# Performance work log

Hardware: AMD Instinct MI355X
Metric: run time of the kernel (lower is better)

The kernel has to match this reference:

```python
import jax, jax.numpy as jnp
from jax import lax
import numpy as np

# dims
B, S, IN, E = 2, 2048, 512, 1024
INNER = 2 * E              # mLSTM up-projection, proj_factor = 2.0
NH = 4                     # mLSTM cell heads
DH = INNER // NH           # 512
QKV_BLK = 4                # qkv_proj_blocksize
NHW = INNER // QKV_BLK     # heads of block-diagonal (headwise) q/k/v projections
K = 4                      # causal conv1d kernel size
EPS = 1e-6                 # mLSTM cell eps
LN_EPS = 1e-5


def setup_inputs() -> dict:
    key = jax.random.key(0)
    ks = jax.random.split(key, 16)
    n = lambda k, shp, s=0.02: jax.random.normal(k, shp, jnp.float32) * s
    z = lambda shp: jnp.zeros(shp, jnp.float32)
    return dict(
        x=jax.random.normal(ks[0], (B, S, IN), jnp.float32),
        w_in=n(ks[1], (IN, E)), b_in=z((E,)),
        ln1_w=jnp.ones((E,), jnp.float32),
        w_up=n(ks[2], (E, 2 * INNER)), b_up=z((2 * INNER,)),
        conv_w=n(ks[3], (INNER, K), 0.1), conv_b=z((INNER,)),
        q_w=n(ks[4], (NHW, QKV_BLK, QKV_BLK), 0.3), q_b=z((INNER,)),
        k_w=n(ks[5], (NHW, QKV_BLK, QKV_BLK), 0.3), k_b=z((INNER,)),
        v_w=n(ks[6], (NHW, QKV_BLK, QKV_BLK), 0.3), v_b=z((INNER,)),
        ig_w=n(ks[7], (3 * INNER, NH)), ig_b=z((NH,)),
        fg_w=n(ks[8], (3 * INNER, NH)), fg_b=jnp.ones((NH,), jnp.float32),
        onorm_w=jnp.ones((INNER,), jnp.float32),
        skip=n(ks[9], (INNER,), 1.0),
        w_down=n(ks[10], (INNER, E)), b_down=z((E,)),
        post_w=jnp.ones((E,), jnp.float32),
    )


def _layernorm(x, w, eps=LN_EPS):
    m = x.mean(-1, keepdims=True)
    v = x.var(-1, keepdims=True)
    return (x - m) / jnp.sqrt(v + eps) * w


def _headwise(x, w, b):
    # block-diagonal linear: x (B,S,INNER) split into NHW blocks of QKV_BLK
    Bx, Sx, _ = x.shape
    y = jnp.einsum('bshd,hod->bsho', x.reshape(Bx, Sx, NHW, QKV_BLK), w)
    return y.reshape(Bx, Sx, INNER) + b


def _mlstm_parallel(q, k, v, ig, fg):
    # q,k,v: (B,NH,S,DH); ig,fg: (B,NH,S). Parallel (stabilized) mLSTM.
    log_f = jax.nn.log_sigmoid(fg)                       # (B,NH,S)
    cum = jnp.cumsum(log_f, axis=-1)                     # inclusive cumsum
    dmat = cum[..., :, None] - cum[..., None, :]         # F_i - F_j  (B,NH,S,S)
    mask = jnp.tril(jnp.ones((S, S), bool))
    logD = jnp.where(mask, dmat + ig[..., None, :], -jnp.inf)
    m = logD.max(-1, keepdims=True)                      # (B,NH,S,1)
    Dm = jnp.exp(logD - m)
    qk = jnp.einsum('bnid,bnjd->bnij', q, k) / jnp.sqrt(jnp.float32(DH))
    C = qk * Dm
    norm = jnp.maximum(jnp.abs(C.sum(-1, keepdims=True)), jnp.exp(-m))
    return jnp.einsum('bnij,bnjd->bnid', C / (norm + EPS), v)


def _forward(x, w_in, b_in, ln1_w, w_up, b_up, conv_w, conv_b,
             q_w, q_b, k_w, k_b, v_w, v_b, ig_w, ig_b, fg_w, fg_b,
             onorm_w, skip, w_down, b_down, post_w):
    h_in = x @ w_in + b_in                               # (B,S,E); dropout = identity (eval)

    # --- mLSTM block: residual + pre-LN ---
    xn = _layernorm(h_in, ln1_w)
    up = xn @ w_up + b_up                                # (B,S,2*INNER)
    x_m, z = jnp.split(up, 2, axis=-1)

    # causal depthwise conv1d + SiLU
    rhs = conv_w.T[:, None, :]                           # (K,1,INNER)
    xc = lax.conv_general_dilated(x_m, rhs, window_strides=(1,),
                                  padding=[(K - 1, 0)],
                                  dimension_numbers=('NHC', 'HIO', 'NHC'),
                                  feature_group_count=INNER) + conv_b
    x_conv_act = jax.nn.silu(xc)

    q = _headwise(x_conv_act, q_w, q_b)                  # (B,S,INNER)
    k = _headwise(x_conv_act, k_w, k_b)
    v = _headwise(x_m, v_w, v_b)

    if_in = jnp.concatenate([q, k, v], axis=-1)          # (B,S,3*INNER)
    ig = (if_in @ ig_w + ig_b).transpose(0, 2, 1)        # (B,NH,S)
    fg = (if_in @ fg_w + fg_b).transpose(0, 2, 1)

    to_heads = lambda t: t.reshape(B, S, NH, DH).transpose(0, 2, 1, 3)
    h = _mlstm_parallel(to_heads(q), to_heads(k), to_heads(v), ig, fg)  # (B,NH,S,DH)

    # multi-head (group) norm over DH, then learned scale over flat features
    hn = (h - h.mean(-1, keepdims=True)) / jnp.sqrt(h.var(-1, keepdims=True) + LN_EPS)
    hn = hn.transpose(0, 2, 1, 3).reshape(B, S, INNER) * onorm_w

    h_skip = hn + skip * x_conv_act                      # learnable skip
    h_gated = h_skip * jax.nn.silu(z)                    # output gate
    y = h_gated @ w_down + b_down                        # (B,S,E)

    out = h_in + y                                       # residual
    return _layernorm(out, post_w)                       # post_blocks_norm


def reference(x, w_in, b_in, ln1_w, w_up, b_up, conv_w, conv_b,
              q_w, q_b, k_w, k_b, v_w, v_b, ig_w, ig_b, fg_w, fg_b,
              onorm_w, skip, w_down, b_down, post_w):
    return _forward(x, w_in, b_in, ln1_w, w_up, b_up, conv_w, conv_b,
                    q_w, q_b, k_w, k_b, v_w, v_b, ig_w, ig_b, fg_w, fg_b,
                    onorm_w, skip, w_down, b_down, post_w)
```

## Files before the change

### kernel.cpp

```cpp
#include <hip/hip_runtime.h>
#include <hip/hip_bf16.h>

typedef __hip_bfloat16 bf16;
typedef float floatx4 __attribute__((ext_vector_type(4)));
typedef short bf16x8 __attribute__((ext_vector_type(8)));

#define B_      2
#define S_      2048
#define IN_     512
#define E_      1024
#define INNER_  2048
#define NH_     4
#define DH_     512
#define T_      (B_*S_)
#define EPS_CELL 1e-6f
#define LN_EPS_  1e-5f
#define LS      72
#define CTB_    4

__device__ inline float b2f(bf16 x){ return __bfloat162float(x); }
__device__ inline bf16  f2b(float x){ return __float2bfloat16(x); }
__device__ inline float u2f(unsigned int u){ union{unsigned int i; float f;} v; v.i = u; return v.f; }
__device__ inline unsigned short f2bu(float x){ bf16 t = __float2bfloat16(x); unsigned short r; __builtin_memcpy(&r,&t,2); return r; }
__device__ inline void unpack8(uint4 u, float* f){
  f[0]=u2f(u.x<<16); f[1]=u2f(u.x&0xffff0000u);
  f[2]=u2f(u.y<<16); f[3]=u2f(u.y&0xffff0000u);
  f[4]=u2f(u.z<<16); f[5]=u2f(u.z&0xffff0000u);
  f[6]=u2f(u.w<<16); f[7]=u2f(u.w&0xffff0000u);
}
__device__ inline uint4 pack8(const float* f){
  uint4 u;
  u.x = (unsigned)f2bu(f[0]) | ((unsigned)f2bu(f[1])<<16);
  u.y = (unsigned)f2bu(f[2]) | ((unsigned)f2bu(f[3])<<16);
  u.z = (unsigned)f2bu(f[4]) | ((unsigned)f2bu(f[5])<<16);
  u.w = (unsigned)f2bu(f[6]) | ((unsigned)f2bu(f[7])<<16);
  return u;
}
__device__ inline void stv(bf16* p, float v){ *p = f2b(v); }
__device__ inline void stv(float* p, float v){ *p = v; }

typedef __attribute__((address_space(3))) unsigned int lds_u32_t;
typedef __attribute__((address_space(1))) const unsigned int glb_u32_t;
__device__ __forceinline__ void cp_async16(const bf16* g, short* l){
  __builtin_amdgcn_global_load_lds((glb_u32_t*)(const void*)g,
                                   (lds_u32_t*)(void*)l, 16, 0, 0);
}
__device__ __forceinline__ int so_(int row, int c8){ return row*64 + (((c8) ^ (row&7))<<3); }
__device__ __forceinline__ int eo_(int row, int ch){ return row*128 + (((ch) ^ (row&15))<<3); }

#define STAGE_ASYNC(dst, srcbase, stride, kk) \
  { int slot_ = (kk)*256 + tid; int r_ = slot_>>3; int c8_ = (slot_&7) ^ (r_&7); \
    cp_async16((srcbase) + (size_t)r_*(stride) + c8_*8, &dst[slot_*8]); }

#define STAGE_ASYNC5(dst, srcbase, stride, kk) \
  { int slot_ = (kk)*512 + tid; int r_ = slot_>>3; int c8_ = (slot_&7) ^ (r_&7); \
    cp_async16((srcbase) + (size_t)r_*(stride) + c8_*8, &dst[slot_*8]); }

#define VMWAIT8() asm volatile("s_waitcnt vmcnt(8)" ::: "memory")
#define VMWAIT6() asm volatile("s_waitcnt vmcnt(6)" ::: "memory")
#define VMWAIT0() asm volatile("s_waitcnt vmcnt(0)" ::: "memory")
#define RAWBAR()  do { asm volatile("" ::: "memory"); __builtin_amdgcn_s_barrier(); asm volatile("" ::: "memory"); } while(0)

__device__ inline void transpose_tile(const float* W, bf16* Wt, int K, int N,
    int n0, int k0, int tid, float (*tl)[65]){
  #pragma unroll
  for (int i=0;i<4;i++){
    int idx = tid + i*256; int r = idx>>4, c4 = idx&15;
    float4 v = *(const float4*)(W + (size_t)(k0+r)*N + n0 + c4*4);
    tl[r][c4*4+0]=v.x; tl[r][c4*4+1]=v.y; tl[r][c4*4+2]=v.z; tl[r][c4*4+3]=v.w;
  }
  __syncthreads();
  #pragma unroll
  for (int i=0;i<4;i++){
    int idx = tid + i*256; int rn = idx>>4, c4 = idx&15;
    ushort4 o;
    o.x=f2bu(tl[c4*4+0][rn]); o.y=f2bu(tl[c4*4+1][rn]);
    o.z=f2bu(tl[c4*4+2][rn]); o.w=f2bu(tl[c4*4+3][rn]);
    *(ushort4*)(Wt + (size_t)(n0+rn)*K + k0 + c4*4) = o;
  }
}

__global__ __launch_bounds__(256) void prep_fused(const float* __restrict__ x,
    const float* __restrict__ w_in, const float* __restrict__ w_up,
    const float* __restrict__ igw, const float* __restrict__ fgw,
    bf16* __restrict__ xbf, bf16* __restrict__ w_in_t, bf16* __restrict__ w_up_t,
    bf16* __restrict__ gwb){
  __shared__ float tl[64][65];
  int bid = blockIdx.x, tid = threadIdx.x;
  if (bid < 1024){
    int i = bid*256 + tid;
    const float4* p = (const float4*)(x) + i*2;
    float4 a = p[0], b = p[1];
    ushort4 o0, o1;
    o0.x=f2bu(a.x); o0.y=f2bu(a.y); o0.z=f2bu(a.z); o0.w=f2bu(a.w);
    o1.x=f2bu(b.x); o1.y=f2bu(b.y); o1.z=f2bu(b.z); o1.w=f2bu(b.w);
    ushort4* q = (ushort4*)(xbf) + i*2;
    q[0]=o0; q[1]=o1;
  } else if (bid < 1152){
    int id = bid - 1024;
    int n0 = (id & 15)*64, k0 = (id >> 4)*64;
    transpose_tile(w_in, w_in_t, IN_, E_, n0, k0, tid, tl);
  } else if (bid < 2176){
    int id = bid - 1152;
    int n0 = (id & 63)*64, k0 = (id >> 6)*64;
    transpose_tile(w_up, w_up_t, E_, 2*INNER_, n0, k0, tid, tl);
  } else {
    int idx = (bid - 2176)*256 + tid;
    if (idx < 3*INNER_){
      int g = idx >> 9;
      int e = (idx >> 6) & 7;
      int l = idx & 63;
      int r = g*512 + l*8 + e;
      float4 a = *(const float4*)(igw + (size_t)r*4);
      float4 b = *(const float4*)(fgw + (size_t)r*4);
      ushort4 o0, o1;
      o0.x=f2bu(a.x); o0.y=f2bu(a.y); o0.z=f2bu(a.z); o0.w=f2bu(a.w);
      o1.x=f2bu(b.x); o1.y=f2bu(b.y); o1.z=f2bu(b.z); o1.w=f2bu(b.w);
      *(ushort4*)(gwb + (size_t)idx*8)     = o0;
      *(ushort4*)(gwb + (size_t)idx*8 + 4) = o1;
    }
  }
}

__global__ __launch_bounds__(256) void mfma_gemm(const bf16* __restrict__ A,
    const bf16* __restrict__ Bt, const float* __restrict__ bias, bf16* __restrict__ C,
    int Kd, int lda, int ldc, int NN){
  int bid = blockIdx.x;
  int MM = gridDim.x / NN;
  int mPerX = MM >> 3;
  int xcd = bid & 7, seq = bid >> 3;
  int nb = seq % NN, mb = xcd*mPerX + seq / NN;
  int n0 = nb*128, m0 = mb*128;
  __shared__ __align__(16) short smem[32768];
  int tid = threadIdx.x;
  int w = tid>>6, l = tid&63, lq = l>>4, lr = l&15;
  int wm = (w>>1)*64, wn = (w&1)*64;
  const bf16* Abase = A + (size_t)m0*lda;
  const bf16* Bbase = Bt + (size_t)n0*Kd;
  floatx4 acc[4][4];
  #pragma unroll
  for (int mi=0;mi<4;mi++){
    #pragma unroll
    for (int ni=0;ni<4;ni++) acc[mi][ni] = (floatx4){0.f,0.f,0.f,0.f};
  }
  short* As0 = smem;          short* Bs0 = smem + 8192;
  short* As1 = smem + 16384;  short* Bs1 = smem + 24576;
  int NT = Kd >> 6;
  #pragma unroll
  for (int kk=0;kk<4;kk++){
    STAGE_ASYNC(As0, Abase, lda, kk);
    STAGE_ASYNC(Bs0, Bbase, Kd, kk);
  }
  #pragma unroll
  for (int kk=0;kk<4;kk++){
    STAGE_ASYNC(As1, Abase + 64, lda, kk);
    STAGE_ASYNC(Bs1, Bbase + 64, Kd, kk);
  }
  for (int t=0; t<NT; ++t){
    if (t < NT-1) { VMWAIT8(); } else { VMWAIT0(); }
    RAWBAR();
    short* As = (t&1) ? As1 : As0;
    short* Bs = (t&1) ? Bs1 : Bs0;
    #pragma unroll
    for (int ks=0; ks<2; ks++){
      bf16x8 af[4], bfr[4];
      #pragma unroll
      for (int mi=0;mi<4;mi++) af[mi] = *(const bf16x8*)&As[so_(wm+mi*16+lr, ks*4+lq)];
      #pragma unroll
      for (int ni=0;ni<4;ni++) bfr[ni] = *(const bf16x8*)&Bs[so_(wn+ni*16+lr, ks*4+lq)];
      #pragma unroll
      for (int mi=0;mi<4;mi++){
        #pragma unroll
        for (int ni=0;ni<4;ni++)
          acc[mi][ni] = __builtin_amdgcn_mfma_f32_16x16x32_bf16(af[mi], bfr[ni], acc[mi][ni], 0,0,0);
      }
    }
    RAWBAR();
    if (t+2 < NT){
      int k0 = (t+2)*64;
      #pragma unroll
      for (int kk=0;kk<4;kk++){
        STAGE_ASYNC(As, Abase + k0, lda, kk);
        STAGE_ASYNC(Bs, Bbase + k0, Kd, kk);
      }
    }
  }
  float bb[4];
  #pragma unroll
  for (int ni=0;ni<4;ni++) bb[ni] = bias[n0 + wn + ni*16 + lr];
  __syncthreads();
  #pragma unroll
  for (int mi=0;mi<4;mi++){
    #pragma unroll
    for (int ni=0;ni<4;ni++){
      int coll = wn + ni*16 + lr;
      int ch = coll>>3, off = coll&7;
      #pragma unroll
      for (int r=0;r<4;r++){
        int rowl = wm + mi*16 + lq*4 + r;
        smem[rowl*128 + (((ch) ^ (rowl&15))<<3) + off] = (short)f2bu(acc[mi][ni][r] + bb[ni]);
      }
    }
  }
  __syncthreads();
  #pragma unroll
  for (int i=0;i<8;i++){
    int slot = i*256 + tid;
    int r = slot >> 4, c8 = slot & 15;
    uint4 val = *(const uint4*)&smem[eo_(r, c8)];
    *(uint4*)(C + (size_t)(m0+r)*ldc + n0 + c8*8) = val;
  }
}

__global__ __launch_bounds__(256) void mfma_gemm64(const bf16* __restrict__ A,
    const bf16* __restrict__ Bt, const float* __restrict__ bias, bf16* __restrict__ C,
    int Kd, int lda, int ldc, int NN){
  int bid = blockIdx.x;
  int MM = gridDim.x / NN;
  int mPerX = MM >> 3;
  int xcd = bid & 7, seq = bid >> 3;
  int nb = seq % NN, mb = xcd*mPerX + seq / NN;
  int n0 = nb*128, m0 = mb*64;
  __shared__ __align__(16) short smem[24576];
  int tid = threadIdx.x;
  int w = tid>>6, l = tid&63, lq = l>>4, lr = l&15;
  int wm = (w>>1)*32, wn = (w&1)*64;
  const bf16* Abase = A + (size_t)m0*lda;
  const bf16* Bbase = Bt + (size_t)n0*Kd;
  floatx4 acc[2][4];
  #pragma unroll
  for (int mi=0;mi<2;mi++){
    #pragma unroll
    for (int ni=0;ni<4;ni++) acc[mi][ni] = (floatx4){0.f,0.f,0.f,0.f};
  }
  short* As0 = smem;          short* Bs0 = smem + 4096;
  short* As1 = smem + 12288;  short* Bs1 = smem + 16384;
  int NT = Kd >> 6;
  STAGE_ASYNC(As0, Abase, lda, 0);
  STAGE_ASYNC(As0, Abase, lda, 1);
  #pragma unroll
  for (int kk=0;kk<4;kk++){ STAGE_ASYNC(Bs0, Bbase, Kd, kk); }
  STAGE_ASYNC(As1, Abase + 64, lda, 0);
  STAGE_ASYNC(As1, Abase + 64, lda, 1);
  #pragma unroll
  for (int kk=0;kk<4;kk++){ STAGE_ASYNC(Bs1, Bbase + 64, Kd, kk); }
  for (int t=0; t<NT; ++t){
    if (t < NT-1) { VMWAIT6(); } else { VMWAIT0(); }
    RAWBAR();
    short* As = (t&1) ? As1 : As0;
    short* Bs = (t&1) ? Bs1 : Bs0;
    #pragma unroll
    for (int ks=0; ks<2; ks++){
      bf16x8 af[2], bfr[4];
      #pragma unroll
      for (int mi=0;mi<2;mi++) af[mi] = *(const bf16x8*)&As[so_(wm+mi*16+lr, ks*4+lq)];
      #pragma unroll
      for (int ni=0;ni<4;ni++) bfr[ni] = *(const bf16x8*)&Bs[so_(wn+ni*16+lr, ks*4+lq)];
      #pragma unroll
      for (int mi=0;mi<2;mi++){
        #pragma unroll
        for (int ni=0;ni<4;ni++)
          acc[mi][ni] = __builtin_amdgcn_mfma_f32_16x16x32_bf16(af[mi], bfr[ni], acc[mi][ni], 0,0,0);
      }
    }
    RAWBAR();
    if (t+2 < NT){
      int k0 = (t+2)*64;
      STAGE_ASYNC(As, Abase + k0, lda, 0);
      STAGE_ASYNC(As, Abase + k0, lda, 1);
      #pragma unroll
      for (int kk=0;kk<4;kk++){ STAGE_ASYNC(Bs, Bbase + k0, Kd, kk); }
    }
  }
  float bb[4];
  #pragma unroll
  for (int ni=0;ni<4;ni++) bb[ni] = bias[n0 + wn + ni*16 + lr];
  __syncthreads();
  #pragma unroll
  for (int mi=0;mi<2;mi++){
    #pragma unroll
    for (int ni=0;ni<4;ni++){
      int coll = wn + ni*16 + lr;
      int ch = coll>>3, off = coll&7;
      #pragma unroll
      for (int r=0;r<4;r++){
        int rowl = wm + mi*16 + lq*4 + r;
        smem[rowl*128 + (((ch) ^ (rowl&15))<<3) + off] = (short)f2bu(acc[mi][ni][r] + bb[ni]);
      }
    }
  }
  __syncthreads();
  #pragma unroll
  for (int i=0;i<4;i++){
    int slot = i*256 + tid;
    int r = slot >> 4, c8 = slot & 15;
    uint4 val = *(const uint4*)&smem[eo_(r, c8)];
    *(uint4*)(C + (size_t)(m0+r)*ldc + n0 + c8*8) = val;
  }
}

template<typename OutT>
__global__ __launch_bounds__(256) void ln_rows(const bf16* __restrict__ X,
    const bf16* __restrict__ Xadd, const float* __restrict__ w, OutT* __restrict__ Y){
  int row = blockIdx.x, tid = threadIdx.x;
  size_t base = (size_t)row*E_;
  float vals[4], s=0.f, s2=0.f;
  #pragma unroll
  for (int e=0;e<4;e++){
    int c = e*256+tid;
    float v = b2f(X[base+c]);
    if (Xadd) v += b2f(Xadd[base+c]);
    vals[e]=v; s+=v; s2+=v*v;
  }
  __shared__ float sa[256], sb[256];
  sa[tid]=s; sb[tid]=s2; __syncthreads();
  for (int off=128; off>0; off>>=1){
    if (tid<off){ sa[tid]+=sa[tid+off]; sb[tid]+=sb[tid+off]; }
    __syncthreads();
  }
  float mean = sa[0]*(1.f/E_);
  float var  = sb[0]*(1.f/E_) - mean*mean;
  float rstd = rsqrtf(var + LN_EPS_);
  #pragma unroll
  for (int e=0;e<4;e++){
    int c = e*256+tid;
    stv(&Y[base+c], (vals[e]-mean)*rstd*w[c]);
  }
}

__global__ __launch_bounds__(256) void conv_headwise(const bf16* __restrict__ up,
    const float* __restrict__ cw, const float* __restrict__ cb,
    const float* __restrict__ qw, const float* __restrict__ qb,
    const float* __restrict__ kw, const float* __restrict__ kb,
    const float* __restrict__ vw, const float* __restrict__ vb,
    bf16* __restrict__ xca, bf16* __restrict__ q, bf16* __restrict__ k,
    bf16* __restrict__ v){
  int t0 = blockIdx.x*CTB_;
  int s0 = t0 & (S_-1);
  int c0 = threadIdx.x*8;
  int hw0 = c0 >> 2;

  float row[7][8];
  #pragma unroll
  for (int j=0;j<7;j++){
    if (s0-3+j >= 0){
      uint4 rv = *(const uint4*)(up + (size_t)(t0-3+j)*(2*INNER_) + c0);
      unpack8(rv, row[j]);
    } else {
      #pragma unroll
      for (int e=0;e<8;e++) row[j][e]=0.f;
    }
  }

  float xc[CTB_][8];
  {
    float cwv[8][4], cbv[8];
    #pragma unroll
    for (int e=0;e<8;e++){
      float4 w4 = *(const float4*)(cw + (size_t)(c0+e)*4);
      cwv[e][0]=w4.x; cwv[e][1]=w4.y; cwv[e][2]=w4.z; cwv[e][3]=w4.w;
    }
    float4 b0 = *(const float4*)(cb+c0), b1 = *(const float4*)(cb+c0+4);
    cbv[0]=b0.x; cbv[1]=b0.y; cbv[2]=b0.z; cbv[3]=b0.w;
    cbv[4]=b1.x; cbv[5]=b1.y; cbv[6]=b1.z; cbv[7]=b1.w;
    #pragma unroll
    for (int i=0;i<CTB_;i++){
      #pragma unroll
      for (int e=0;e<8;e++){
        float a = cbv[e];
        #pragma unroll
        for (int t=0;t<4;t++) a += row[i+t][e]*cwv[e][t];
        xc[i][e] = a/(1.f+expf(-a));
      }
      *(uint4*)(xca + (size_t)(t0+i)*INNER_ + c0) = pack8(xc[i]);
    }
  }

  {
    float wv_[32], bv[8];
    #pragma unroll
    for (int g=0;g<2;g++){
      #pragma unroll
      for (int r4=0;r4<4;r4++){
        float4 w4 = *(const float4*)(vw + (size_t)(hw0+g)*16 + r4*4);
        wv_[g*16+r4*4+0]=w4.x; wv_[g*16+r4*4+1]=w4.y;
        wv_[g*16+r4*4+2]=w4.z; wv_[g*16+r4*4+3]=w4.w;
      }
    }
    float4 b0 = *(const float4*)(vb+c0), b1 = *(const float4*)(vb+c0+4);
    bv[0]=b0.x; bv[1]=b0.y; bv[2]=b0.z; bv[3]=b0.w;
    bv[4]=b1.x; bv[5]=b1.y; bv[6]=b1.z; bv[7]=b1.w;
    #pragma unroll
    for (int i=0;i<CTB_;i++){
      float ov[8];
      #pragma unroll
      for (int g=0;g<2;g++){
        #pragma unroll
        for (int o=0;o<4;o++){
          float a = bv[g*4+o];
          #pragma unroll
          for (int d=0;d<4;d++) a += row[i+3][g*4+d]*wv_[g*16+o*4+d];
          ov[g*4+o]=a;
        }
      }
      *(uint4*)(v + (size_t)(t0+i)*INNER_ + c0) = pack8(ov);
    }
  }

  {
    float wv_[32], bv[8];
    #pragma unroll
    for (int g=0;g<2;g++){
      #pragma unroll
      for (int r4=0;r4<4;r4++){
        float4 w4 = *(const float4*)(qw + (size_t)(hw0+g)*16 + r4*4);
        wv_[g*16+r4*4+0]=w4.x; wv_[g*16+r4*4+1]=w4.y;
        wv_[g*16+r4*4+2]=w4.z; wv_[g*16+r4*4+3]=w4.w;
      }
    }
    float4 b0 = *(const float4*)(qb+c0), b1 = *(const float4*)(qb+c0+4);
    bv[0]=b0.x; bv[1]=b0.y; bv[2]=b0.z; bv[3]=b0.w;
    bv[4]=b1.x; bv[5]=b1.y; bv[6]=b1.z; bv[7]=b1.w;
    #pragma unroll
    for (int i=0;i<CTB_;i++){
      float ov[8];
      #pragma unroll
      for (int g=0;g<2;g++){
        #pragma unroll
        for (int o=0;o<4;o++){
          float a = bv[g*4+o];
          #pragma unroll
          for (int d=0;d<4;d++) a += xc[i][g*4+d]*wv_[g*16+o*4+d];
          ov[g*4+o]=a;
        }
      }
      *(uint4*)(q + (size_t)(t0+i)*INNER_ + c0) = pack8(ov);
    }
  }

  {
    float wv_[32], bv[8];
    #pragma unroll
    for (int g=0;g<2;g++){
      #pragma unroll
      for (int r4=0;r4<4;r4++){
        float4 w4 = *(const float4*)(kw + (size_t)(hw0+g)*16 + r4*4);
        wv_[g*16+r4*4+0]=w4.x; wv_[g*16+r4*4+1]=w4.y;
        wv_[g*16+r4*4+2]=w4.z; wv_[g*16+r4*4+3]=w4.w;
      }
    }
    float4 b0 = *(const float4*)(kb+c0), b1 = *(const float4*)(kb+c0+4);
    bv[0]=b0.x; bv[1]=b0.y; bv[2]=b0.z; bv[3]=b0.w;
    bv[4]=b1.x; bv[5]=b1.y; bv[6]=b1.z; bv[7]=b1.w;
    #pragma unroll
    for (int i=0;i<CTB_;i++){
      float ov[8];
      #pragma unroll
      for (int g=0;g<2;g++){
        #pragma unroll
        for (int o=0;o<4;o++){
          float a = bv[g*4+o];
          #pragma unroll
          for (int d=0;d<4;d++) a += xc[i][g*4+d]*wv_[g*16+o*4+d];
          ov[g*4+o]=a;
        }
      }
      *(uint4*)(k + (size_t)(t0+i)*INNER_ + c0) = pack8(ov);
    }
  }
}

__global__ __launch_bounds__(256) void gates_transv(const bf16* __restrict__ q,
    const bf16* __restrict__ k, const bf16* __restrict__ v,
    const bf16* __restrict__ gwb, const float* __restrict__ igb,
    const float* __restrict__ fgb, float* __restrict__ igo, float* __restrict__ fgo,
    bf16* __restrict__ vT){
  __shared__ float red[4*32];
  __shared__ short tl[64*LS];
  int bid = blockIdx.x, tid = threadIdx.x;
  if (bid < 512){
    int w = tid >> 6, l = tid & 63;
    int quad = w >> 1, kh = w & 1;
    int tok0 = bid*8 + quad*4;
    float acc[4][8];
    #pragma unroll
    for (int t=0;t<4;t++){
      #pragma unroll
      for (int n=0;n<8;n++) acc[t][n]=0.f;
    }
    #pragma unroll 2
    for (int it=0; it<6; ++it){
      int src = it >> 1, j = it & 1;
      const bf16* sp = (src==0) ? q : ((src==1) ? k : v);
      int pos = kh*1024 + j*512 + l*8;
      int g = src*4 + kh*2 + j;
      uint4 dv[4];
      #pragma unroll
      for (int t=0;t<4;t++)
        dv[t] = *(const uint4*)(sp + (size_t)(tok0+t)*INNER_ + pos);
      float d[4][8];
      #pragma unroll
      for (int t=0;t<4;t++) unpack8(dv[t], d[t]);
      const bf16* wb = gwb + (size_t)g*512*8;
      #pragma unroll
      for (int e=0;e<8;e++){
        uint4 wv = *(const uint4*)(wb + (size_t)(e*64 + l)*8);
        float w8[8]; unpack8(wv, w8);
        #pragma unroll
        for (int t=0;t<4;t++){
          #pragma unroll
          for (int n=0;n<8;n++) acc[t][n] += d[t][e]*w8[n];
        }
      }
    }
    #pragma unroll
    for (int off=1; off<64; off<<=1){
      #pragma unroll
      for (int t=0;t<4;t++){
        #pragma unroll
        for (int n=0;n<8;n++) acc[t][n] += __shfl_xor(acc[t][n], off);
      }
    }
    if (l == 0){
      #pragma unroll
      for (int t=0;t<4;t++){
        #pragma unroll
        for (int n=0;n<8;n++) red[w*32 + t*8 + n] = acc[t][n];
      }
    }
    __syncthreads();
    if (tid < 64){
      int qd = tid >> 5, tn = tid & 31;
      int t = tn >> 3, n = tn & 7;
      float val = red[(qd*2)*32 + tn] + red[(qd*2+1)*32 + tn];
      int tok = bid*8 + qd*4 + t;
      int b = tok >> 11, s = tok & (S_-1);
      if (n < 4) igo[((size_t)(b*NH_+n))*S_ + s] = val + igb[n];
      else       fgo[((size_t)(b*NH_+(n-4)))*S_ + s] = val + fgb[n-4];
    }
  } else {
    int id = bid - 512;
    int sb = id & 31, db = (id >> 5) & 7, h = id >> 8;
    int b = h >> 2, n = h & 3;
    int s0 = sb*64, d0 = db*64;
    #pragma unroll
    for (int i=0;i<2;i++){
      int vv = tid + i*256; int r = vv>>3, c8 = vv&7;
      uint4 x = *(const uint4*)(v + (size_t)(b*S_+s0+r)*INNER_ + n*DH_ + d0 + c8*8);
      *(uint4*)&tl[r*LS + c8*8] = x;
    }
    __syncthreads();
    #pragma unroll
    for (int i=0;i<2;i++){
      int vv = tid + i*256; int r = vv>>3, c8 = vv&7;
      unsigned short tmp[8];
      #pragma unroll
      for (int e=0;e<8;e++) tmp[e] = (unsigned short)tl[(c8*8+e)*LS + r];
      uint4 o; __builtin_memcpy(&o, tmp, 16);
      *(uint4*)(vT + ((size_t)h*DH_ + d0 + r)*S_ + s0 + c8*8) = o;
    }
  }
}

__global__ __launch_bounds__(256) void scan8(const float* __restrict__ igp,
    const float* __restrict__ fgp, float* __restrict__ ap,
    float* __restrict__ Mp, float* __restrict__ flp, float* __restrict__ rowsum){
  int h = blockIdx.x, tid = threadIdx.x;
  const float* fg = fgp + (size_t)h*S_;
  const float* ig = igp + (size_t)h*S_;
  int base = tid*8;
  float loc[8], run = 0.f;
  #pragma unroll
  for (int e=0;e<8;e++){
    float x = fg[base+e];
    float ls = fminf(x,0.f) - log1pf(expf(-fabsf(x)));
    run += ls; loc[e] = run;
  }
  __shared__ float sd[256];
  sd[tid]=run; __syncthreads();
  if (tid==0){ float r=0.f; for(int t=0;t<256;t++){ float t0=sd[t]; sd[t]=r; r+=t0; } }
  __syncthreads();
  float off = sd[tid];
  float lm[8], rm = -3e38f;
  #pragma unroll
  for (int e=0;e<8;e++){
    float F = loc[e]+off; loc[e]=F;
    float aj = ig[base+e]-F;
    ap[(size_t)h*S_+base+e]=aj;
    rm = fmaxf(rm, aj); lm[e]=rm;
  }
  __syncthreads();
  sd[tid]=rm; __syncthreads();
  if (tid==0){ float r=-3e38f; for(int t=0;t<256;t++){ float t0=sd[t]; sd[t]=r; r=fmaxf(r,t0); } }
  __syncthreads();
  float offm = sd[tid];
  #pragma unroll
  for (int e=0;e<8;e++){
    float M = fmaxf(lm[e], offm);
    Mp[(size_t)h*S_+base+e]=M;
    flp[(size_t)h*S_+base+e]=expf(-loc[e]-M);
    rowsum[(size_t)h*S_+base+e]=0.f;
  }
}

__global__ __launch_bounds__(512) void qk_decay_kernel(const bf16* __restrict__ qg,
    const bf16* __restrict__ kg, const float* __restrict__ ap,
    const float* __restrict__ Mp, float* __restrict__ rowsum, bf16* __restrict__ W){
  int h = blockIdx.x & 7;
  int t = 271 - (blockIdx.x >> 3);
  int p = (int)((sqrtf(4.f*t+1.f)-1.f)*0.5f);
  while ((p+1)*(p+2) <= t) p++;
  while (p*(p+1) > t) p--;
  int r0 = t - p*(p+1);
  int nj = p + 1;
  int it = 2*p + (r0 >= nj ? 1 : 0);
  int tj = r0 >= nj ? r0 - nj : r0;
  int b = h >> 2, n = h & 3;
  int i0 = it*64, j0 = tj*128;
  __shared__ __align__(16) short smem[2*12288];
  __shared__ float a_s[128], m_s[64];
  int tid = threadIdx.x;
  if (tid < 128) a_s[tid] = ap[(size_t)h*S_ + j0 + tid];
  if (tid < 64)  m_s[tid] = Mp[(size_t)h*S_ + i0 + tid];
  int w = tid>>6, l = tid&63, lq = l>>4, lr = l&15;
  int wm = (w>>1)*16, wn = (w&1)*64;
  const bf16* Qbase = qg + (size_t)(b*S_+i0)*INNER_ + n*DH_;
  const bf16* Kbase = kg + (size_t)(b*S_+j0)*INNER_ + n*DH_;
  floatx4 acc[4];
  #pragma unroll
  for (int ni=0;ni<4;ni++) acc[ni] = (floatx4){0.f,0.f,0.f,0.f};
  short* Qs0 = smem;          short* Ks0 = smem + 4096;
  short* Qs1 = smem + 12288;  short* Ks1 = smem + 16384;
  STAGE_ASYNC5(Qs0, Qbase, INNER_, 0);
  STAGE_ASYNC5(Ks0, Kbase, INNER_, 0);
  STAGE_ASYNC5(Ks0, Kbase, INNER_, 1);
  __syncthreads();
  const int NT = DH_/64;
  for (int tt=0; tt<NT; ++tt){
    short* Qs  = (tt&1) ? Qs1 : Qs0;
    short* Ks  = (tt&1) ? Ks1 : Ks0;
    short* Qsn = (tt&1) ? Qs0 : Qs1;
    short* Ksn = (tt&1) ? Ks0 : Ks1;
    if (tt+1 < NT){
      int d0 = (tt+1)*64;
      STAGE_ASYNC5(Qsn, Qbase + d0, INNER_, 0);
      STAGE_ASYNC5(Ksn, Kbase + d0, INNER_, 0);
      STAGE_ASYNC5(Ksn, Kbase + d0, INNER_, 1);
    }
    #pragma unroll
    for (int ks=0; ks<2; ks++){
      bf16x8 af, bfr[4];
      af = *(const bf16x8*)&Qs[so_(wm+lr, ks*4+lq)];
      #pragma unroll
      for (int ni=0;ni<4;ni++) bfr[ni] = *(const bf16x8*)&Ks[so_(wn+ni*16+lr, ks*4+lq)];
      #pragma unroll
      for (int ni=0;ni<4;ni++)
        acc[ni] = __builtin_amdgcn_mfma_f32_16x16x32_bf16(af, bfr[ni], acc[ni], 0,0,0);
    }
    __syncthreads();
  }
  const float scale = 0.04419417382415922f;
  float rpart[4];
  #pragma unroll
  for (int r=0;r<4;r++) rpart[r]=0.f;
  #pragma unroll
  for (int ni=0;ni<4;ni++){
    int coll = wn + ni*16 + lr;
    int ch = coll>>3, off = coll&7;
    float av = a_s[coll];
    #pragma unroll
    for (int r=0;r<4;r++){
      int rowl = wm + lq*4 + r;
      int gi = i0 + rowl, gj = j0 + coll;
      float wv = 0.f;
      if (gj <= gi) wv = acc[ni][r]*scale*__expf(av-m_s[rowl]);
      smem[rowl*128 + (((ch) ^ (rowl&15))<<3) + off] = (short)f2bu(wv);
      rpart[r] += wv;
    }
  }
  __syncthreads();
  #pragma unroll
  for (int i=0;i<2;i++){
    int slot = i*512 + tid;
    int r = slot >> 4, c8 = slot & 15;
    uint4 val = *(const uint4*)&smem[eo_(r, c8)];
    *(uint4*)(W + ((size_t)h*S_ + i0 + r)*S_ + j0 + c8*8) = val;
  }
  #pragma unroll
  for (int r=0;r<4;r++){
    float v = rpart[r];
    v += __shfl_xor(v, 1, 16);
    v += __shfl_xor(v, 2, 16);
    v += __shfl_xor(v, 4, 16);
    v += __shfl_xor(v, 8, 16);
    if (lr == 0)
      atomicAdd(&rowsum[(size_t)h*S_ + i0 + wm + lq*4 + r], v);
  }
}

__global__ __launch_bounds__(512) void pv_kernel(const bf16* __restrict__ W,
    const bf16* __restrict__ vT, const float* __restrict__ rowsum,
    const float* __restrict__ fl, bf16* __restrict__ O){
  int h = blockIdx.x & 7;
  int s = blockIdx.x >> 3;
  int ti = 31 - (s >> 2), tn = s & 3;
  int b = h >> 2, n = h & 3;
  int i0 = ti*64, d0 = tn*128;
  __shared__ __align__(16) short smem[2*12288];
  __shared__ float inv_s[64];
  int tid = threadIdx.x;
  if (tid < 64){
    size_t o = (size_t)h*S_ + i0 + tid;
    inv_s[tid] = 1.f/(fmaxf(fabsf(rowsum[o]), fl[o]) + EPS_CELL);
  }
  int w = tid>>6, l = tid&63, lq = l>>4, lr = l&15;
  int wm = (w>>1)*16, wn = (w&1)*64;
  const bf16* Wbase = W + ((size_t)h*S_ + i0)*S_;
  const bf16* Vbase = vT + ((size_t)h*DH_ + d0)*S_;
  floatx4 acc[4];
  #pragma unroll
  for (int ni=0;ni<4;ni++) acc[ni] = (floatx4){0.f,0.f,0.f,0.f};
  short* Ws0 = smem;          short* Vs0 = smem + 4096;
  short* Ws1 = smem + 12288;  short* Vs1 = smem + 16384;
  int NT = (i0 >> 6) + 1;
  STAGE_ASYNC5(Ws0, Wbase, S_, 0);
  STAGE_ASYNC5(Vs0, Vbase, S_, 0);
  STAGE_ASYNC5(Vs0, Vbase, S_, 1);
  __syncthreads();
  for (int tt=0; tt<NT; ++tt){
    short* Ws  = (tt&1) ? Ws1 : Ws0;
    short* Vs  = (tt&1) ? Vs1 : Vs0;
    short* Wsn = (tt&1) ? Ws0 : Ws1;
    short* Vsn = (tt&1) ? Vs0 : Vs1;
    if (tt+1 < NT){
      int j0 = (tt+1)*64;
      STAGE_ASYNC5(Wsn, Wbase + j0, S_, 0);
      STAGE_ASYNC5(Vsn, Vbase + j0, S_, 0);
      STAGE_ASYNC5(Vsn, Vbase + j0, S_, 1);
    }
    #pragma unroll
    for (int ks=0; ks<2; ks++){
      bf16x8 af, bfr[4];
      af = *(const bf16x8*)&Ws[so_(wm+lr, ks*4+lq)];
      #pragma unroll
      for (int ni=0;ni<4;ni++) bfr[ni] = *(const bf16x8*)&Vs[so_(wn+ni*16+lr, ks*4+lq)];
      #pragma unroll
      for (int ni=0;ni<4;ni++)
        acc[ni] = __builtin_amdgcn_mfma_f32_16x16x32_bf16(af, bfr[ni], acc[ni], 0,0,0);
    }
    __syncthreads();
  }
  #pragma unroll
  for (int ni=0;ni<4;ni++){
    int dl = wn + ni*16 + lr;
    int ch = dl>>3, off = dl&7;
    #pragma unroll
    for (int r=0;r<4;r++){
      int rowl = wm + lq*4 + r;
      smem[rowl*128 + (((ch) ^ (rowl&15))<<3) + off] = (short)f2bu(acc[ni][r] * inv_s[rowl]);
    }
  }
  __syncthreads();
  #pragma unroll
  for (int i=0;i<2;i++){
    int slot = i*512 + tid;
    int r = slot >> 4, c8 = slot & 15;
    uint4 val = *(const uint4*)&smem[eo_(r, c8)];
    *(uint4*)(O + (size_t)(b*S_ + i0 + r)*INNER_ + n*DH_ + d0 + c8*8) = val;
  }
}

__global__ __launch_bounds__(256) void headnorm_wdown(const bf16* __restrict__ h,
    const float* __restrict__ onw, const float* __restrict__ skip,
    const bf16* __restrict__ xca, bf16* __restrict__ up,
    const float* __restrict__ w_down, bf16* __restrict__ w_down_t){
  __shared__ float sa[256], sb[256];
  __shared__ float tl[64][65];
  int bid = blockIdx.x, tid = threadIdx.x;
  if (bid < 512){
    int n0 = (bid & 15)*64, k0 = (bid >> 4)*64;
    transpose_tile(w_down, w_down_t, INNER_, E_, n0, k0, tid, tl);
    return;
  }
  int id = bid - 512;
  int n = id & 3; int bs = id >> 2;
  size_t hbase = (size_t)bs*INNER_ + n*DH_;
  float v0 = b2f(h[hbase+tid]);
  float v1 = b2f(h[hbase+256+tid]);
  sa[tid]=v0+v1; sb[tid]=v0*v0+v1*v1;
  __syncthreads();
  for (int off=128; off>0; off>>=1){
    if (tid<off){ sa[tid]+=sa[tid+off]; sb[tid]+=sb[tid+off]; }
    __syncthreads();
  }
  float mean = sa[0]*(1.f/DH_);
  float var  = sb[0]*(1.f/DH_) - mean*mean;
  float rstd = rsqrtf(var + LN_EPS_);
  #pragma unroll
  for (int e=0;e<2;e++){
    int dl = e*256+tid; int c = n*DH_+dl;
    float hv = e ? v1 : v0;
    float hn = (hv-mean)*rstd*onw[c];
    float hs = hn + skip[c]*b2f(xca[(size_t)bs*INNER_+c]);
    size_t zoff = (size_t)bs*(2*INNER_) + INNER_ + c;
    float zv = b2f(up[zoff]);
    float sz = zv/(1.f+expf(-zv));
    up[zoff] = f2b(hs*sz);
  }
}

extern "C" void kernel_launch(void* const* d_in, const int* in_sizes, int n_in,
                              void* d_out, int out_size, void* d_ws, size_t ws_size,
                              hipStream_t stream) {
  const float* x      = (const float*)d_in[0];
  const float* w_in   = (const float*)d_in[1];
  const float* b_in   = (const float*)d_in[2];
  const float* ln1_w  = (const float*)d_in[3];
  const float* w_up   = (const float*)d_in[4];
  const float* b_up   = (const float*)d_in[5];
  const float* conv_w = (const float*)d_in[6];
  const float* conv_b = (const float*)d_in[7];
  const float* q_w    = (const float*)d_in[8];
  const float* q_b    = (const float*)d_in[9];
  const float* k_w    = (const float*)d_in[10];
  const float* k_b    = (const float*)d_in[11];
  const float* v_w    = (const float*)d_in[12];
  const float* v_b    = (const float*)d_in[13];
  const float* ig_w   = (const float*)d_in[14];
  const float* ig_b   = (const float*)d_in[15];
  const float* fg_w   = (const float*)d_in[16];
  const float* fg_b   = (const float*)d_in[17];
  const float* onw    = (const float*)d_in[18];
  const float* skip   = (const float*)d_in[19];
  const float* w_down = (const float*)d_in[20];
  const float* b_down = (const float*)d_in[21];
  const float* post_w = (const float*)d_in[22];

  char* p = (char*)d_ws;
  auto alloc = [&](size_t bytes)->void*{ void* r = p; p += (bytes + 255) & ~(size_t)255; return r; };
  bf16* h_in = (bf16*)alloc((size_t)T_*E_*2);
  bf16* xn   = (bf16*)alloc((size_t)T_*E_*2);
  bf16* up   = (bf16*)alloc((size_t)T_*2*INNER_*2);
  bf16* xca  = (bf16*)alloc((size_t)T_*INNER_*2);
  bf16* qb_  = (bf16*)alloc((size_t)T_*INNER_*2);
  bf16* kb_  = (bf16*)alloc((size_t)T_*INNER_*2);
  bf16* vb_  = (bf16*)alloc((size_t)T_*INNER_*2);
  bf16* hb_  = (bf16*)alloc((size_t)T_*INNER_*2);
  float* igbuf = (float*)alloc((size_t)B_*NH_*S_*4);
  float* fgbuf = (float*)alloc((size_t)B_*NH_*S_*4);
  float* abuf  = (float*)alloc((size_t)B_*NH_*S_*4);
  float* Mbuf  = (float*)alloc((size_t)B_*NH_*S_*4);
  float* flbuf = (float*)alloc((size_t)B_*NH_*S_*4);
  float* rsbuf = (float*)alloc((size_t)B_*NH_*S_*4);
  bf16* gwb  = (bf16*)alloc((size_t)3*INNER_*8*2);
  bf16* Wbuf = (bf16*)alloc((size_t)B_*NH_*S_*S_*2);
  bf16* ybuf = xn;
  bf16* vTb  = hb_;
  bf16* obuf = vb_;
  bf16* xbf    = Wbuf;
  bf16* w_in_t = Wbuf + (size_t)T_*IN_;
  bf16* w_up_t = w_in_t + (size_t)E_*IN_;
  bf16* w_down_t = Wbuf;

  prep_fused<<<2200, 256, 0, stream>>>(x, w_in, w_up, ig_w, fg_w,
      xbf, w_in_t, w_up_t, gwb);
  mfma_gemm64<<<(T_/64)*(E_/128), 256, 0, stream>>>(xbf, w_in_t, b_in, h_in, IN_, IN_, E_, E_/128);
  ln_rows<bf16><<<T_, 256, 0, stream>>>(h_in, nullptr, ln1_w, xn);
  mfma_gemm<<<(T_/128)*((2*INNER_)/128), 256, 0, stream>>>(xn, w_up_t, b_up, up, E_, E_, 2*INNER_, (2*INNER_)/128);
  conv_headwise<<<T_/CTB_, 256, 0, stream>>>(up, conv_w, conv_b,
      q_w, q_b, k_w, k_b, v_w, v_b, xca, qb_, kb_, vb_);
  gates_transv<<<512 + 2048, 256, 0, stream>>>(qb_, kb_, vb_, gwb, ig_b, fg_b,
      igbuf, fgbuf, vTb);
  scan8<<<B_*NH_, 256, 0, stream>>>(igbuf, fgbuf, abuf, Mbuf, flbuf, rsbuf);
  qk_decay_kernel<<<8*272, 512, 0, stream>>>(qb_, kb_, abuf, Mbuf, rsbuf, Wbuf);
  pv_kernel<<<8*128, 512, 0, stream>>>(Wbuf, vTb, rsbuf, flbuf, obuf);
  headnorm_wdown<<<512 + T_*NH_, 256, 0, stream>>>(obuf, onw, skip, xca, up,
      w_down, w_down_t);
  mfma_gemm64<<<(T_/64)*(E_/128), 256, 0, stream>>>(up + INNER_, w_down_t, b_down, ybuf, INNER_, 2*INNER_, E_, E_/128);
  ln_rows<float><<<T_, 256, 0, stream>>>(h_in, ybuf, post_w, (float*)d_out);
}
```

Baseline: 357.4 us.

## Fuse decay-weighted QK and PV into a single flash-style attention kernel

Replaces the two-pass scheme that wrote a full S×S decay-weighted score matrix to global memory, then multiplied it by V, with one kernel per (head, 64-row query tile). Q stays in registers, K and V chunks stream through LDS, and row sums are reduced in-block instead of with atomics. This removes the large intermediate traffic and a kernel launch. The trade-off is only 256 blocks with causal load imbalance and heavy LDS use per block.

```diff
diff --git a/kernel.cpp b/kernel.cpp
--- a/kernel.cpp
+++ b/kernel.cpp
@@ -52,9 +52,9 @@
   { int slot_ = (kk)*256 + tid; int r_ = slot_>>3; int c8_ = (slot_&7) ^ (r_&7); \
     cp_async16((srcbase) + (size_t)r_*(stride) + c8_*8, &dst[slot_*8]); }
 
-#define STAGE_ASYNC5(dst, srcbase, stride, kk) \
-  { int slot_ = (kk)*512 + tid; int r_ = slot_>>3; int c8_ = (slot_&7) ^ (r_&7); \
-    cp_async16((srcbase) + (size_t)r_*(stride) + c8_*8, &dst[slot_*8]); }
+#define STAGE_CH(dst, src, stride) \
+  { int r_ = tid>>3; int c8_ = (tid&7) ^ (r_&7); \
+    cp_async16((src) + (size_t)r_*(stride) + c8_*8, (dst) + tid*8); }
 
 #define VMWAIT8() asm volatile("s_waitcnt vmcnt(8)" ::: "memory")
 #define VMWAIT6() asm volatile("s_waitcnt vmcnt(6)" ::: "memory")
@@ -603,170 +603,165 @@
   }
 }
 
-__global__ __launch_bounds__(512) void qk_decay_kernel(const bf16* __restrict__ qg,
-    const bf16* __restrict__ kg, const float* __restrict__ ap,
-    const float* __restrict__ Mp, float* __restrict__ rowsum, bf16* __restrict__ W){
+__global__ __launch_bounds__(512) void attn_fused(const bf16* __restrict__ qg,
+    const bf16* __restrict__ kg, const bf16* __restrict__ vT,
+    const float* __restrict__ ap, const float* __restrict__ Mp,
+    const float* __restrict__ fl, bf16* __restrict__ O){
   int h = blockIdx.x & 7;
-  int t = 271 - (blockIdx.x >> 3);
-  int p = (int)((sqrtf(4.f*t+1.f)-1.f)*0.5f);
-  while ((p+1)*(p+2) <= t) p++;
-  while (p*(p+1) > t) p--;
-  int r0 = t - p*(p+1);
-  int nj = p + 1;
-  int it = 2*p + (r0 >= nj ? 1 : 0);
-  int tj = r0 >= nj ? r0 - nj : r0;
+  int ti = 31 - (blockIdx.x >> 3);
   int b = h >> 2, n = h & 3;
-  int i0 = it*64, j0 = tj*128;
-  __shared__ __align__(16) short smem[2*12288];
-  __shared__ float a_s[128], m_s[64];
+  int i0 = ti*64;
+  __shared__ __align__(16) short Ks[32768];
+  __shared__ __align__(16) short Vs[32768];
+  __shared__ __align__(16) short Ss[4096];
+  __shared__ float rsP[8][16];
+  __shared__ float inv_s[64];
   int tid = threadIdx.x;
-  if (tid < 128) a_s[tid] = ap[(size_t)h*S_ + j0 + tid];
-  if (tid < 64)  m_s[tid] = Mp[(size_t)h*S_ + i0 + tid];
   int w = tid>>6, l = tid&63, lq = l>>4, lr = l&15;
-  int wm = (w>>1)*16, wn = (w&1)*64;
-  const bf16* Qbase = qg + (size_t)(b*S_+i0)*INNER_ + n*DH_;
-  const bf16* Kbase = kg + (size_t)(b*S_+j0)*INNER_ + n*DH_;
-  floatx4 acc[4];
-  #pragma unroll
-  for (int ni=0;ni<4;ni++) acc[ni] = (floatx4){0.f,0.f,0.f,0.f};
-  short* Qs0 = smem;          short* Ks0 = smem + 4096;
-  short* Qs1 = smem + 12288;  short* Ks1 = smem + 16384;
-  STAGE_ASYNC5(Qs0, Qbase, INNER_, 0);
-  STAGE_ASYNC5(Ks0, Kbase, INNER_, 0);
-  STAGE_ASYNC5(Ks0, Kbase, INNER_, 1);
-  __syncthreads();
-  const int NT = DH_/64;
-  for (int tt=0; tt<NT; ++tt){
-    short* Qs  = (tt&1) ? Qs1 : Qs0;
-    short* Ks  = (tt&1) ? Ks1 : Ks0;
-    short* Qsn = (tt&1) ? Qs0 : Qs1;
-    short* Ksn = (tt&1) ? Ks0 : Ks1;
-    if (tt+1 < NT){
-      int d0 = (tt+1)*64;
-      STAGE_ASYNC5(Qsn, Qbase + d0, INNER_, 0);
-      STAGE_ASYNC5(Ksn, Kbase + d0, INNER_, 0);
-      STAGE_ASYNC5(Ksn, Kbase + d0, INNER_, 1);
-    }
+  int fi = w>>1;
+  int jh = w&1;
+  const float scale = 0.04419417382415922f;
+
+  const bf16* Qrow = qg + (size_t)(b*S_ + i0 + fi*16 + lr)*INNER_ + n*DH_;
+  bf16x8 qreg[16];
+  #pragma unroll
+  for (int m=0;m<16;m++)
+    qreg[m] = *(const bf16x8*)(Qrow + m*32 + lq*8);
+  float mrow[4];
+  #pragma unroll
+  for (int r=0;r<4;r++)
+    mrow[r] = Mp[(size_t)h*S_ + i0 + fi*16 + lq*4 + r];
+
+  floatx4 acc[4][4];
+  #pragma unroll
+  for (int mi=0;mi<4;mi++){
+    #pragma unroll
+    for (int ni=0;ni<4;ni++) acc[mi][ni] = (floatx4){0.f,0.f,0.f,0.f};
+  }
+  float rpart[2][4];
+  #pragma unroll
+  for (int f=0;f<2;f++){
+    #pragma unroll
+    for (int r=0;r<4;r++) rpart[f][r]=0.f;
+  }
+  const bf16* Kbase = kg + (size_t)(b*S_)*INNER_ + n*DH_;
+  const bf16* Vbase = vT + (size_t)h*DH_*S_;
+
+  #pragma unroll
+  for (int c=0;c<8;c++){
+    STAGE_CH(&Ks[c*4096], Kbase + c*64, INNER_);
+  }
+  __syncthreads();
+
+  int NT = ti + 1;
+  for (int j=0; j<NT; ++j){
+    int j0 = j*64;
+    #pragma unroll
+    for (int c=0;c<8;c++){
+      STAGE_CH(&Vs[c*4096], Vbase + (size_t)(c*64)*S_ + j0, S_);
+    }
+    floatx4 sacc[2];
+    sacc[0] = (floatx4){0.f,0.f,0.f,0.f};
+    sacc[1] = (floatx4){0.f,0.f,0.f,0.f};
+    #pragma unroll
+    for (int dc=0; dc<8; dc++){
+      #pragma unroll
+      for (int ks=0; ks<2; ks++){
+        bf16x8 bf0 = *(const bf16x8*)&Ks[dc*4096 + so_(jh*32 + lr, ks*4+lq)];
+        bf16x8 bf1 = *(const bf16x8*)&Ks[dc*4096 + so_(jh*32 + 16 + lr, ks*4+lq)];
+        sacc[0] = __builtin_amdgcn_mfma_f32_16x16x32_bf16(qreg[dc*2+ks], bf0, sacc[0], 0,0,0);
+        sacc[1] = __builtin_amdgcn_mfma_f32_16x16x32_bf16(qreg[dc*2+ks], bf1, sacc[1], 0,0,0);
+      }
+    }
+    float a0 = ap[(size_t)h*S_ + j0 + jh*32 + lr];
+    float a1 = ap[(size_t)h*S_ + j0 + jh*32 + 16 + lr];
+    #pragma unroll
+    for (int fjt=0; fjt<2; fjt++){
+      int col = jh*32 + fjt*16 + lr;
+      int gj = j0 + col;
+      float av = fjt ? a1 : a0;
+      int ch = col>>3, off = col&7;
+      #pragma unroll
+      for (int r=0;r<4;r++){
+        int row = fi*16 + lq*4 + r;
+        int gi = i0 + row;
+        float wv = 0.f;
+        if (gj <= gi) wv = sacc[fjt][r]*scale*__expf(av - mrow[r]);
+        Ss[row*64 + (((ch) ^ (row&7))<<3) + off] = (short)f2bu(wv);
+        rpart[fjt][r] += wv;
+      }
+    }
+    __syncthreads();
+    if (j+1 < NT){
+      int jn = j0 + 64;
+      #pragma unroll
+      for (int c=0;c<8;c++){
+        STAGE_CH(&Ks[c*4096], Kbase + (size_t)jn*INNER_ + c*64, INNER_);
+      }
+    }
+    const short* VsW = Vs + w*4096;
     #pragma unroll
     for (int ks=0; ks<2; ks++){
-      bf16x8 af, bfr[4];
-      af = *(const bf16x8*)&Qs[so_(wm+lr, ks*4+lq)];
-      #pragma unroll
-      for (int ni=0;ni<4;ni++) bfr[ni] = *(const bf16x8*)&Ks[so_(wn+ni*16+lr, ks*4+lq)];
-      #pragma unroll
-      for (int ni=0;ni<4;ni++)
-        acc[ni] = __builtin_amdgcn_mfma_f32_16x16x32_bf16(af, bfr[ni], acc[ni], 0,0,0);
+      bf16x8 af[4], bfv[4];
+      #pragma unroll
+      for (int mi=0;mi<4;mi++) af[mi] = *(const bf16x8*)&Ss[so_(mi*16+lr, ks*4+lq)];
+      #pragma unroll
+      for (int ni=0;ni<4;ni++) bfv[ni] = *(const bf16x8*)&VsW[so_(ni*16+lr, ks*4+lq)];
+      #pragma unroll
+      for (int mi=0;mi<4;mi++){
+        #pragma unroll
+        for (int ni=0;ni<4;ni++)
+          acc[mi][ni] = __builtin_amdgcn_mfma_f32_16x16x32_bf16(af[mi], bfv[ni], acc[mi][ni], 0,0,0);
+      }
     }
     __syncthreads();
   }
-  const float scale = 0.04419417382415922f;
-  float rpart[4];
-  #pragma unroll
-  for (int r=0;r<4;r++) rpart[r]=0.f;
-  #pragma unroll
-  for (int ni=0;ni<4;ni++){
-    int coll = wn + ni*16 + lr;
-    int ch = coll>>3, off = coll&7;
-    float av = a_s[coll];
-    #pragma unroll
-    for (int r=0;r<4;r++){
-      int rowl = wm + lq*4 + r;
-      int gi = i0 + rowl, gj = j0 + coll;
-      float wv = 0.f;
-      if (gj <= gi) wv = acc[ni][r]*scale*__expf(av-m_s[rowl]);
-      smem[rowl*128 + (((ch) ^ (rowl&15))<<3) + off] = (short)f2bu(wv);
-      rpart[r] += wv;
-    }
-  }
-  __syncthreads();
-  #pragma unroll
-  for (int i=0;i<2;i++){
-    int slot = i*512 + tid;
-    int r = slot >> 4, c8 = slot & 15;
-    uint4 val = *(const uint4*)&smem[eo_(r, c8)];
-    *(uint4*)(W + ((size_t)h*S_ + i0 + r)*S_ + j0 + c8*8) = val;
-  }
+
+  float rs[4];
   #pragma unroll
   for (int r=0;r<4;r++){
-    float v = rpart[r];
+    float v = rpart[0][r] + rpart[1][r];
     v += __shfl_xor(v, 1, 16);
     v += __shfl_xor(v, 2, 16);
     v += __shfl_xor(v, 4, 16);
     v += __shfl_xor(v, 8, 16);
-    if (lr == 0)
-      atomicAdd(&rowsum[(size_t)h*S_ + i0 + wm + lq*4 + r], v);
-  }
-}
-
-__global__ __launch_bounds__(512) void pv_kernel(const bf16* __restrict__ W,
-    const bf16* __restrict__ vT, const float* __restrict__ rowsum,
-    const float* __restrict__ fl, bf16* __restrict__ O){
-  int h = blockIdx.x & 7;
-  int s = blockIdx.x >> 3;
-  int ti = 31 - (s >> 2), tn = s & 3;
-  int b = h >> 2, n = h & 3;
-  int i0 = ti*64, d0 = tn*128;
-  __shared__ __align__(16) short smem[2*12288];
-  __shared__ float inv_s[64];
-  int tid = threadIdx.x;
+    rs[r] = v;
+  }
+  if (lr == 0){
+    #pragma unroll
+    for (int r=0;r<4;r++) rsP[w][lq*4+r] = rs[r];
+  }
+  __syncthreads();
   if (tid < 64){
-    size_t o = (size_t)h*S_ + i0 + tid;
-    inv_s[tid] = 1.f/(fmaxf(fabsf(rowsum[o]), fl[o]) + EPS_CELL);
-  }
-  int w = tid>>6, l = tid&63, lq = l>>4, lr = l&15;
-  int wm = (w>>1)*16, wn = (w&1)*64;
-  const bf16* Wbase = W + ((size_t)h*S_ + i0)*S_;
-  const bf16* Vbase = vT + ((size_t)h*DH_ + d0)*S_;
-  floatx4 acc[4];
-  #pragma unroll
-  for (int ni=0;ni<4;ni++) acc[ni] = (floatx4){0.f,0.f,0.f,0.f};
-  short* Ws0 = smem;          short* Vs0 = smem + 4096;
-  short* Ws1 = smem + 12288;  short* Vs1 = smem + 16384;
-  int NT = (i0 >> 6) + 1;
-  STAGE_ASYNC5(Ws0, Wbase, S_, 0);
-  STAGE_ASYNC5(Vs0, Vbase, S_, 0);
-  STAGE_ASYNC5(Vs0, Vbase, S_, 1);
-  __syncthreads();
-  for (int tt=0; tt<NT; ++tt){
-    short* Ws  = (tt&1) ? Ws1 : Ws0;
-    short* Vs  = (tt&1) ? Vs1 : Vs0;
-    short* Wsn = (tt&1) ? Ws0 : Ws1;
-    short* Vsn = (tt&1) ? Vs0 : Vs1;
-    if (tt+1 < NT){
-      int j0 = (tt+1)*64;
-      STAGE_ASYNC5(Wsn, Wbase + j0, S_, 0);
-      STAGE_ASYNC5(Vsn, Vbase + j0, S_, 0);
-      STAGE_ASYNC5(Vsn, Vbase + j0, S_, 1);
-    }
-    #pragma unroll
-    for (int ks=0; ks<2; ks++){
-      bf16x8 af, bfr[4];
-      af = *(const bf16x8*)&Ws[so_(wm+lr, ks*4+lq)];
-      #pragma unroll
-      for (int ni=0;ni<4;ni++) bfr[ni] = *(const bf16x8*)&Vs[so_(wn+ni*16+lr, ks*4+lq)];
-      #pragma unroll
-      for (int ni=0;ni<4;ni++)
-        acc[ni] = __builtin_amdgcn_mfma_f32_16x16x32_bf16(af, bfr[ni], acc[ni], 0,0,0);
-    }
-    __syncthreads();
-  }
-  #pragma unroll
-  for (int ni=0;ni<4;ni++){
-    int dl = wn + ni*16 + lr;
-    int ch = dl>>3, off = dl&7;
-    #pragma unroll
-    for (int r=0;r<4;r++){
-      int rowl = wm + lq*4 + r;
-      smem[rowl*128 + (((ch) ^ (rowl&15))<<3) + off] = (short)f2bu(acc[ni][r] * inv_s[rowl]);
-    }
-  }
-  __syncthreads();
-  #pragma unroll
-  for (int i=0;i<2;i++){
-    int slot = i*512 + tid;
-    int r = slot >> 4, c8 = slot & 15;
-    uint4 val = *(const uint4*)&smem[eo_(r, c8)];
-    *(uint4*)(O + (size_t)(b*S_ + i0 + r)*INNER_ + n*DH_ + d0 + c8*8) = val;
+    int fi2 = tid>>4, rl = tid&15;
+    float rsum = rsP[fi2*2][rl] + rsP[fi2*2+1][rl];
+    inv_s[tid] = 1.f/(fmaxf(fabsf(rsum), fl[(size_t)h*S_ + i0 + tid]) + EPS_CELL);
+  }
+  __syncthreads();
+  {
+    short* Od = Ks + w*4096;
+    #pragma unroll
+    for (int mi=0;mi<4;mi++){
+      #pragma unroll
+      for (int ni=0;ni<4;ni++){
+        int col = ni*16 + lr;
+        int ch = col>>3, off = col&7;
+        #pragma unroll
+        for (int r=0;r<4;r++){
+          int row = mi*16 + lq*4 + r;
+          Od[row*64 + (((ch) ^ (row&7))<<3) + off] = (short)f2bu(acc[mi][ni][r] * inv_s[row]);
+        }
+      }
+    }
+  }
+  __syncthreads();
+  #pragma unroll
+  for (int it=0; it<8; ++it){
+    int slot = it*512 + tid;
+    int r = slot >> 6, cg = slot & 63;
+    int wch = cg >> 3, c8 = cg & 7;
+    uint4 val = *(const uint4*)&Ks[wch*4096 + so_(r, c8)];
+    *(uint4*)(O + (size_t)(b*S_ + i0 + r)*INNER_ + n*DH_ + wch*64 + c8*8) = val;
   }
 }
 
@@ -872,8 +867,7 @@
   gates_transv<<<512 + 2048, 256, 0, stream>>>(qb_, kb_, vb_, gwb, ig_b, fg_b,
       igbuf, fgbuf, vTb);
   scan8<<<B_*NH_, 256, 0, stream>>>(igbuf, fgbuf, abuf, Mbuf, flbuf, rsbuf);
-  qk_decay_kernel<<<8*272, 512, 0, stream>>>(qb_, kb_, abuf, Mbuf, rsbuf, Wbuf);
-  pv_kernel<<<8*128, 512, 0, stream>>>(Wbuf, vTb, rsbuf, flbuf, obuf);
+  attn_fused<<<256, 512, 0, stream>>>(qb_, kb_, vTb, abuf, Mbuf, flbuf, obuf);
   headnorm_wdown<<<512 + T_*NH_, 256, 0, stream>>>(obuf, onw, skip, xca, up,
       w_down, w_down_t);
   mfma_gemm64<<<(T_/64)*(E_/128), 256, 0, stream>>>(up + INNER_, w_down_t, b_down, ybuf, INNER_, 2*INNER_, E_, E_/128);
```

Measured after the change: 390.2 us. +9.2%, slower.
